# Kernel tuning notes

Hardware: AMD Instinct MI355X
Metric: run time of the kernel (lower is better)

Reference implementation:

```python
import jax, jax.numpy as jnp
import numpy as np

N, E, G = 50000, 800000, 1000
F, FM, L, H, T = 128, 16, 7, 128, 12
DIN, DH = 2 * F + 1, 2 * (2 * F + 1)  # 257, 514
UIN, UH = F + FM, 2 * F               # 144, 256

def swish(x):
    return x * jax.nn.sigmoid(x)

def setup_inputs() -> dict:
    key = jax.random.key(0)
    ks = jax.random.split(key, 16)
    pos = jax.random.normal(ks[0], (N, 3), dtype=jnp.float32)
    zi = jax.random.randint(ks[1], (N,), 0, 5)
    z = jnp.array([1, 6, 7, 8, 9], dtype=jnp.int64)[zi]  # valid atomic numbers
    edge_index = jax.random.randint(ks[2], (2, E), 0, N)
    batch = jnp.sort(jax.random.randint(ks[3], (N,), 0, G))
    def w(k, shape, fan_in):
        return jax.random.normal(k, shape, dtype=jnp.float32) / np.sqrt(fan_in)
    return {
        'pos': pos, 'z': z, 'edge_index': edge_index, 'batch': batch,
        'emb': jax.random.normal(ks[4], (5, F), dtype=jnp.float32),
        'W_msg1': w(ks[5], (L, DIN, DH), DIN), 'b_msg1': jnp.zeros((L, DH), jnp.float32),
        'W_msg2': w(ks[6], (L, DH, FM), DH), 'b_msg2': jnp.zeros((L, FM), jnp.float32),
        'W_up1': w(ks[7], (L, UIN, UH), UIN), 'b_up1': jnp.zeros((L, UH), jnp.float32),
        'W_up2': w(ks[8], (L, UH, F), UH), 'b_up2': jnp.zeros((L, F), jnp.float32),
        'Wp1': w(ks[9], (F, H), F), 'bp1': jnp.zeros((H,), jnp.float32),
        'Wp2': w(ks[10], (H, H), H), 'bp2': jnp.zeros((H,), jnp.float32),
        'Wr1': w(ks[11], (H, H), H), 'br1': jnp.zeros((H,), jnp.float32),
        'Wr2': w(ks[12], (H, T), H), 'br2': jnp.zeros((T,), jnp.float32),
        'n_graphs': G,
    }

def reference(pos, z, edge_index, batch, emb, W_msg1, b_msg1, W_msg2, b_msg2,
              W_up1, b_up1, W_up2, b_up2, Wp1, bp1, Wp2, bp2, Wr1, br1, Wr2, br2,
              n_graphs):
    n = pos.shape[0]
    atomic = jnp.array([-1, 0, -1, -1, -1, -1, 1, 2, 3, 4])
    h = emb[atomic[z]]                                  # [N, F]
    src, dst = edge_index[0], edge_index[1]
    d = pos[src] - pos[dst]
    norm2 = jnp.sum(d * d, axis=1)                      # [E] squared distance
    for l in range(W_msg1.shape[0]):
        inp = jnp.concatenate([h[dst], h[src], norm2[:, None]], axis=1)  # x_i, x_j, norm2
        m = swish(inp @ W_msg1[l] + b_msg1[l])
        m = swish(m @ W_msg2[l] + b_msg2[l])            # [E, FM]
        agg = jax.ops.segment_sum(m, dst, num_segments=n)  # aggregate at target nodes
        u = jnp.concatenate([agg, h], axis=1)           # [N, F+FM]
        u = swish(u @ W_up1[l] + b_up1[l])
        h = u @ W_up2[l] + b_up2[l] + h                 # residual update
    proj = swish(h @ Wp1 + bp1) @ Wp2 + bp2             # node_proj
    pooled = jax.ops.segment_sum(proj, batch, num_segments=n_graphs)  # global_add_pool
    return swish(pooled @ Wr1 + br1) @ Wr2 + br2        # readout [G, T]
```

## Files before the change

kernel.cpp:

```cpp
#include <hip/hip_runtime.h>
#include <hip/hip_bf16.h>
#include <cstdint>
#include <cstddef>

typedef _Float16 h16x8 __attribute__((ext_vector_type(8)));
typedef float f32x4 __attribute__((ext_vector_type(4)));

#define NSTRIPE 4

__device__ __forceinline__ void splitf16(float v, _Float16& hi, _Float16& lo) {
    hi = (_Float16)v;
    lo = (_Float16)(v - (float)hi);
}
__device__ __forceinline__ float swish_fast(float x) {
    float e = __expf(-x);
    return x * __builtin_amdgcn_rcpf(1.0f + e);
}

__global__ void init_nodes(const int* __restrict__ z, const float* __restrict__ emb,
                           float* __restrict__ hf, _Float16* __restrict__ hhi,
                           _Float16* __restrict__ hlo, int N) {
    int tid = blockIdx.x * 256 + threadIdx.x;
    int n = tid >> 7, f = tid & 127;
    int zv = z[n];
    int idx5 = (zv == 1) ? 0 : (zv - 5);
    float v = emb[idx5 * 128 + f];
    hf[tid] = v;
    _Float16 hi, lo;
    splitf16(v, hi, lo);
    hhi[tid] = hi;
    hlo[tid] = lo;
}

__device__ __forceinline__ int edge_key(int d, int s, int N, int stripeSz) {
    return (d / stripeSz) * N + s;
}

__global__ void hist_kernel(const int* __restrict__ src, const int* __restrict__ dst,
                            int* __restrict__ hist, int E, int N, int stripeSz) {
    int e = blockIdx.x * 256 + threadIdx.x;
    if (e < E) atomicAdd(&hist[edge_key(dst[e], src[e], N, stripeSz)], 1);
}

__global__ void scan_p1(const int* __restrict__ hist, int* __restrict__ blocksum, int KN) {
    __shared__ int s[256];
    int idx = blockIdx.x * 256 + threadIdx.x;
    int v = (idx < KN) ? hist[idx] : 0;
    s[threadIdx.x] = v;
    __syncthreads();
    for (int d = 128; d > 0; d >>= 1) {
        if (threadIdx.x < d) s[threadIdx.x] += s[threadIdx.x + d];
        __syncthreads();
    }
    if (threadIdx.x == 0) blocksum[blockIdx.x] = s[0];
}

__global__ void scan_p2(int* __restrict__ blocksum, int NB) {
    __shared__ int s[1024];
    int t = threadIdx.x;
    int v = (t < NB) ? blocksum[t] : 0;
    s[t] = v;
    __syncthreads();
    for (int d = 1; d < 1024; d <<= 1) {
        int x = (t >= d) ? s[t - d] : 0;
        __syncthreads();
        s[t] += x;
        __syncthreads();
    }
    if (t < NB) blocksum[t] = s[t] - v;
}

__global__ void scan_p3(const int* __restrict__ hist, const int* __restrict__ blocksum,
                        int* __restrict__ cursor, int KN) {
    __shared__ int s[256];
    int idx = blockIdx.x * 256 + threadIdx.x;
    int v = (idx < KN) ? hist[idx] : 0;
    s[threadIdx.x] = v;
    __syncthreads();
    for (int d = 1; d < 256; d <<= 1) {
        int x = (threadIdx.x >= d) ? s[threadIdx.x - d] : 0;
        __syncthreads();
        s[threadIdx.x] += x;
        __syncthreads();
    }
    if (idx < KN) cursor[idx] = blocksum[blockIdx.x] + s[threadIdx.x] - v;
}

__global__ void scatter_kernel(const int* __restrict__ src, const int* __restrict__ dst,
                               int* __restrict__ cursor, int* __restrict__ perm,
                               int E, int N, int stripeSz) {
    int e = blockIdx.x * 256 + threadIdx.x;
    if (e < E) {
        int p = atomicAdd(&cursor[edge_key(dst[e], src[e], N, stripeSz)], 1);
        perm[p] = e;
    }
}

__global__ void reorder_kernel(const int* __restrict__ perm, const int* __restrict__ src,
                               const int* __restrict__ dst, const float* __restrict__ pos,
                               int* __restrict__ srcS, int* __restrict__ dstS,
                               float* __restrict__ n2S, int E) {
    int i = blockIdx.x * 256 + threadIdx.x;
    if (i >= E) return;
    int e = perm[i];
    int si = src[e], di = dst[e];
    srcS[i] = si;
    dstS[i] = di;
    float dx = pos[si * 3 + 0] - pos[di * 3 + 0];
    float dy = pos[si * 3 + 1] - pos[di * 3 + 1];
    float dz = pos[si * 3 + 2] - pos[di * 3 + 2];
    n2S[i] = dx * dx + dy * dy + dz * dz;
}

__global__ void pack_msg1(const float* __restrict__ Wm1l, const float* __restrict__ bm1l,
                          const float* __restrict__ Wm2l,
                          _Float16* __restrict__ Bp1, float* __restrict__ bias1088,
                          _Float16* __restrict__ w1c, _Float16* __restrict__ W2p) {
    int t = blockIdx.x * 256 + threadIdx.x;
    int i = t & 7;
    int lane = (t >> 3) & 63;
    int rest = t >> 9;
    int cb = rest % 68;
    int ks = rest / 68;
    int k = ks * 32 + ((lane >> 4) << 3) + i;
    int ch = cb * 16 + (lane & 15);
    float val;
    if (ch < 544) {
        val = (ch < 514) ? Wm1l[k * 514 + ch] : 0.f;
    } else {
        int c = ch - 544;
        val = (c < 514) ? Wm1l[(128 + k) * 514 + c] : 0.f;
    }
    Bp1[t] = (_Float16)val;
    if (t < 1088) bias1088[t] = (t < 514) ? bm1l[t] : 0.f;
    if (t < 544) w1c[t] = (_Float16)((t < 514) ? Wm1l[256 * 514 + t] : 0.f);
    if (t < 8704) {
        int i2 = t & 7, lane2 = (t >> 3) & 63, ks2 = t >> 9;
        int k2 = ks2 * 32 + ((lane2 >> 4) << 3) + i2;
        int c2 = lane2 & 15;
        W2p[t] = (_Float16)((k2 < 514) ? Wm2l[k2 * 16 + c2] : 0.f);
    }
}

__global__ void pack_generic(const float* __restrict__ W, int K, int Nc,
                             _Float16* __restrict__ Bp) {
    int t = blockIdx.x * 256 + threadIdx.x;
    int i = t & 7;
    int lane = (t >> 3) & 63;
    int rest = t >> 9;
    int CB = Nc >> 4;
    int cb = rest % CB;
    int ks = rest / CB;
    int k = ks * 32 + ((lane >> 4) << 3) + i;
    int c = cb * 16 + (lane & 15);
    float val = (k < K) ? W[(size_t)k * Nc + c] : 0.f;
    Bp[t] = (_Float16)val;
}

__global__ __launch_bounds__(256) void tab_gemm(
    const _Float16* __restrict__ Ahi, const _Float16* __restrict__ Alo,
    const _Float16* __restrict__ Bp, const float* __restrict__ bias,
    _Float16* __restrict__ TA, _Float16* __restrict__ TB, int N) {
    int lane = threadIdx.x & 63;
    int wid = threadIdx.x >> 6;
    int row0 = blockIdx.x * 64 + wid * 16;
    if (row0 >= N) return;
    const size_t arow = (size_t)(row0 + (lane & 15)) * 128;
    const int ak = (lane >> 4) * 8;
    h16x8 ah[4], al[4];
#pragma unroll
    for (int ks = 0; ks < 4; ++ks) {
        ah[ks] = *(const h16x8*)(Ahi + arow + ks * 32 + ak);
        al[ks] = *(const h16x8*)(Alo + arow + ks * 32 + ak);
    }
    int col16 = lane & 15;
    int rb = (lane >> 4) * 4;
    for (int cb = 0; cb < 68; ++cb) {
        f32x4 acc = {0.f, 0.f, 0.f, 0.f};
#pragma unroll
        for (int ks = 0; ks < 4; ++ks) {
            h16x8 bh = *(const h16x8*)(Bp + ((size_t)(ks * 68 + cb) * 64 + lane) * 8);
            acc = __builtin_amdgcn_mfma_f32_16x16x32_f16(ah[ks], bh, acc, 0, 0, 0);
            acc = __builtin_amdgcn_mfma_f32_16x16x32_f16(al[ks], bh, acc, 0, 0, 0);
        }
        int col = cb * 16 + col16;
        float bv = bias[col];
        if (cb < 34) {
#pragma unroll
            for (int i = 0; i < 4; ++i)
                TA[(size_t)(row0 + rb + i) * 544 + col] = (_Float16)(acc[i] + bv);
        } else {
#pragma unroll
            for (int i = 0; i < 4; ++i)
                TB[(size_t)(row0 + rb + i) * 544 + (col - 544)] = (_Float16)(acc[i] + bv);
        }
    }
}

template <int KS, int CB, int MODE>
__global__ __launch_bounds__(256) void gemmA(
    const _Float16* __restrict__ Ahi, const _Float16* __restrict__ Alo, int lda,
    const _Float16* __restrict__ Bp, const float* __restrict__ bias,
    _Float16* __restrict__ outB, _Float16* __restrict__ outB2, int ldoB,
    float* __restrict__ outF, int ldoF, const float* __restrict__ resid,
    const int* __restrict__ batch, float* __restrict__ pooled, int N) {
    int lane = threadIdx.x & 63;
    int wid = threadIdx.x >> 6;
    int row0 = blockIdx.x * 64 + wid * 16;
    if (row0 >= N) return;
    const size_t arow = (size_t)(row0 + (lane & 15)) * lda;
    const int ak = (lane >> 4) * 8;
    h16x8 ah[KS], al[KS];
#pragma unroll
    for (int ks = 0; ks < KS; ++ks) {
        ah[ks] = *(const h16x8*)(Ahi + arow + ks * 32 + ak);
        al[ks] = *(const h16x8*)(Alo + arow + ks * 32 + ak);
    }
    int col16 = lane & 15;
    int rb = (lane >> 4) * 4;
    for (int cb = 0; cb < CB; ++cb) {
        f32x4 acc = {0.f, 0.f, 0.f, 0.f};
#pragma unroll
        for (int ks = 0; ks < KS; ++ks) {
            h16x8 bh = *(const h16x8*)(Bp + ((size_t)(ks * CB + cb) * 64 + lane) * 8);
            acc = __builtin_amdgcn_mfma_f32_16x16x32_f16(ah[ks], bh, acc, 0, 0, 0);
            acc = __builtin_amdgcn_mfma_f32_16x16x32_f16(al[ks], bh, acc, 0, 0, 0);
        }
        int col = cb * 16 + col16;
        float bv = bias[col];
#pragma unroll
        for (int i = 0; i < 4; ++i) {
            int row = row0 + rb + i;
            float v = acc[i] + bv;
            if (MODE == 1) {
                float s = swish_fast(v);
                _Float16 hi, lo;
                splitf16(s, hi, lo);
                outB[(size_t)row * ldoB + col] = hi;
                outB2[(size_t)row * ldoB + col] = lo;
            } else if (MODE == 2) {
                float h = v + resid[(size_t)row * ldoF + col];
                outF[(size_t)row * ldoF + col] = h;
                _Float16 hi, lo;
                splitf16(h, hi, lo);
                outB[(size_t)row * ldoB + col] = hi;
                outB2[(size_t)row * ldoB + col] = lo;
            } else {
                unsafeAtomicAdd(&pooled[(size_t)batch[row] * 128 + col], v);
            }
        }
    }
}

__global__ __launch_bounds__(256) void up1_gemm(
    const float* __restrict__ agg, const float* __restrict__ hf,
    const _Float16* __restrict__ Bp, const float* __restrict__ bias,
    _Float16* __restrict__ uhi, _Float16* __restrict__ ulo, int N) {
    int lane = threadIdx.x & 63;
    int wid = threadIdx.x >> 6;
    int row0 = blockIdx.x * 64 + wid * 16;
    if (row0 >= N) return;
    int r = row0 + (lane & 15);
    const int ak = (lane >> 4) * 8;
    h16x8 ah[5], al[5];
#pragma unroll
    for (int ks = 0; ks < 5; ++ks) {
        int c0 = ks * 32 + ak;
        f32x4 v0, v1;
        if (c0 < 16) {
            v0 = *(const f32x4*)(agg + (size_t)r * 16 + c0);
            v1 = *(const f32x4*)(agg + (size_t)r * 16 + c0 + 4);
        } else if (c0 < 144) {
            v0 = *(const f32x4*)(hf + (size_t)r * 128 + c0 - 16);
            v1 = *(const f32x4*)(hf + (size_t)r * 128 + c0 - 12);
        } else {
            v0 = f32x4{0.f, 0.f, 0.f, 0.f};
            v1 = f32x4{0.f, 0.f, 0.f, 0.f};
        }
        h16x8 hi8, lo8;
#pragma unroll
        for (int jj = 0; jj < 8; ++jj) {
            float x = (jj < 4) ? v0[jj] : v1[jj - 4];
            _Float16 h, l;
            splitf16(x, h, l);
            hi8[jj] = h;
            lo8[jj] = l;
        }
        ah[ks] = hi8;
        al[ks] = lo8;
    }
    int col16 = lane & 15;
    int rb = (lane >> 4) * 4;
    for (int cb = 0; cb < 16; ++cb) {
        f32x4 acc = {0.f, 0.f, 0.f, 0.f};
#pragma unroll
        for (int ks = 0; ks < 5; ++ks) {
            h16x8 bh = *(const h16x8*)(Bp + ((size_t)(ks * 16 + cb) * 64 + lane) * 8);
            acc = __builtin_amdgcn_mfma_f32_16x16x32_f16(ah[ks], bh, acc, 0, 0, 0);
            acc = __builtin_amdgcn_mfma_f32_16x16x32_f16(al[ks], bh, acc, 0, 0, 0);
        }
        int col = cb * 16 + col16;
        float bv = bias[col];
#pragma unroll
        for (int i = 0; i < 4; ++i) {
            int row = row0 + rb + i;
            float s = swish_fast(acc[i] + bv);
            _Float16 hi, lo;
            splitf16(s, hi, lo);
            uhi[(size_t)row * 256 + col] = hi;
            ulo[(size_t)row * 256 + col] = lo;
        }
    }
}

__global__ __launch_bounds__(256) void edge_kernel(
    const _Float16* __restrict__ TA, const _Float16* __restrict__ TB,
    const _Float16* __restrict__ w1c, const _Float16* __restrict__ W2p,
    const float* __restrict__ bm2l,
    const int* __restrict__ srcS, const int* __restrict__ dstS,
    const float* __restrict__ n2S, float* __restrict__ agg) {
    __shared__ _Float16 sW[8704];
    __shared__ _Float16 sw1[544];
    for (int t = threadIdx.x; t < 1088; t += 256)
        ((h16x8*)sW)[t] = ((const h16x8*)W2p)[t];
    for (int t = threadIdx.x; t < 544; t += 256) sw1[t] = w1c[t];
    __syncthreads();

    int lane = threadIdx.x & 63;
    int wid = threadIdx.x >> 6;
    int ebase = blockIdx.x * 128 + wid * 32;
    int rr = lane & 15;
    int e0 = ebase + rr;
    int e1 = ebase + 16 + rr;
    int di0 = dstS[e0], si0 = srcS[e0];
    int di1 = dstS[e1], si1 = srcS[e1];
    _Float16 n20 = (_Float16)n2S[e0];
    _Float16 n21 = (_Float16)n2S[e1];
    const int ak = (lane >> 4) * 8;
    const _Float16* pa0 = TA + (size_t)di0 * 544 + ak;
    const _Float16* pb0 = TB + (size_t)si0 * 544 + ak;
    const _Float16* pa1 = TA + (size_t)di1 * 544 + ak;
    const _Float16* pb1 = TB + (size_t)si1 * 544 + ak;

    const _Float16 nl2e = (_Float16)(-1.44269504f);
    f32x4 acc0 = {0.f, 0.f, 0.f, 0.f};
    f32x4 acc1 = {0.f, 0.f, 0.f, 0.f};

    h16x8 bufA[16], bufB[16], bufT[4];

    auto issue4 = [&](h16x8* buf, int K) {
#pragma unroll
        for (int q = 0; q < 4; ++q) {
            buf[q * 4 + 0] = *(const h16x8*)(pa0 + (K + q) * 32);
            buf[q * 4 + 1] = *(const h16x8*)(pb0 + (K + q) * 32);
            buf[q * 4 + 2] = *(const h16x8*)(pa1 + (K + q) * 32);
            buf[q * 4 + 3] = *(const h16x8*)(pb1 + (K + q) * 32);
        }
    };
    auto step = [&](const h16x8* buf, int q, int ks) {
        h16x8 va0 = buf[q * 4 + 0], vb0 = buf[q * 4 + 1];
        h16x8 va1 = buf[q * 4 + 2], vb1 = buf[q * 4 + 3];
        h16x8 wv = *(const h16x8*)(sw1 + ks * 32 + ak);
        h16x8 x0 = va0 + vb0 + wv * n20;
        h16x8 ev0 = __builtin_elementwise_exp2(x0 * nl2e);
        h16x8 d0 = ev0 + (_Float16)1.0f;
        h16x8 r0;
#pragma unroll
        for (int j = 0; j < 8; ++j) r0[j] = __builtin_amdgcn_rcph(d0[j]);
        h16x8 m0 = x0 * r0;
        h16x8 x1 = va1 + vb1 + wv * n21;
        h16x8 ev1 = __builtin_elementwise_exp2(x1 * nl2e);
        h16x8 d1 = ev1 + (_Float16)1.0f;
        h16x8 r1;
#pragma unroll
        for (int j = 0; j < 8; ++j) r1[j] = __builtin_amdgcn_rcph(d1[j]);
        h16x8 m1 = x1 * r1;
        h16x8 bh = *(const h16x8*)(sW + (ks * 64 + lane) * 8);
        acc0 = __builtin_amdgcn_mfma_f32_16x16x32_f16(m0, bh, acc0, 0, 0, 0);
        acc1 = __builtin_amdgcn_mfma_f32_16x16x32_f16(m1, bh, acc1, 0, 0, 0);
    };

    issue4(bufA, 0);
    __builtin_amdgcn_sched_barrier(0);
    issue4(bufB, 4);
    __builtin_amdgcn_sched_barrier(0);
#pragma unroll
    for (int q = 0; q < 4; ++q) step(bufA, q, q);
    issue4(bufA, 8);
    __builtin_amdgcn_sched_barrier(0);
#pragma unroll
    for (int q = 0; q < 4; ++q) step(bufB, q, 4 + q);
    issue4(bufB, 12);
    __builtin_amdgcn_sched_barrier(0);
#pragma unroll
    for (int q = 0; q < 4; ++q) step(bufA, q, 8 + q);
    bufT[0] = *(const h16x8*)(pa0 + 16 * 32);
    bufT[1] = *(const h16x8*)(pb0 + 16 * 32);
    bufT[2] = *(const h16x8*)(pa1 + 16 * 32);
    bufT[3] = *(const h16x8*)(pb1 + 16 * 32);
    __builtin_amdgcn_sched_barrier(0);
#pragma unroll
    for (int q = 0; q < 4; ++q) step(bufB, q, 12 + q);
    step(bufT, 0, 16);

    int col = lane & 15;
    float b2 = bm2l[col];
#pragma unroll
    for (int i = 0; i < 4; ++i) {
        int ea = ebase + (lane >> 4) * 4 + i;
        float v0 = swish_fast(acc0[i] + b2);
        unsafeAtomicAdd(&agg[(size_t)dstS[ea] * 16 + col], v0);
        int eb = ea + 16;
        float v1 = swish_fast(acc1[i] + b2);
        unsafeAtomicAdd(&agg[(size_t)dstS[eb] * 16 + col], v1);
    }
}

__global__ void readout(const float* __restrict__ pooled, const float* __restrict__ Wr1,
                        const float* __restrict__ br1, const float* __restrict__ Wr2,
                        const float* __restrict__ br2, float* __restrict__ out) {
    __shared__ float row[128];
    __shared__ float tt[128];
    int g = blockIdx.x;
    int t = threadIdx.x;
    row[t] = pooled[g * 128 + t];
    __syncthreads();
    float s = br1[t];
    for (int k = 0; k < 128; ++k) s += row[k] * Wr1[k * 128 + t];
    tt[t] = swish_fast(s);
    __syncthreads();
    if (t < 12) {
        float o = br2[t];
        for (int j = 0; j < 128; ++j) o += tt[j] * Wr2[j * 12 + t];
        out[g * 12 + t] = o;
    }
}

extern "C" void kernel_launch(void* const* d_in, const int* in_sizes, int n_in,
                              void* d_out, int out_size, void* d_ws, size_t ws_size,
                              hipStream_t stream) {
    const float* pos = (const float*)d_in[0];
    const int* z = (const int*)d_in[1];
    const int* ei = (const int*)d_in[2];
    const int* batch = (const int*)d_in[3];
    const float* emb = (const float*)d_in[4];
    const float* Wm1 = (const float*)d_in[5];
    const float* bm1 = (const float*)d_in[6];
    const float* Wm2 = (const float*)d_in[7];
    const float* bm2 = (const float*)d_in[8];
    const float* Wu1 = (const float*)d_in[9];
    const float* bu1 = (const float*)d_in[10];
    const float* Wu2 = (const float*)d_in[11];
    const float* bu2 = (const float*)d_in[12];
    const float* Wp1 = (const float*)d_in[13];
    const float* bp1v = (const float*)d_in[14];
    const float* Wp2 = (const float*)d_in[15];
    const float* bp2v = (const float*)d_in[16];
    const float* Wr1 = (const float*)d_in[17];
    const float* br1 = (const float*)d_in[18];
    const float* Wr2 = (const float*)d_in[19];
    const float* br2 = (const float*)d_in[20];

    const int N = in_sizes[0] / 3;
    const int E = in_sizes[2] / 2;
    const int G = out_size / 12;
    const int* src = ei;
    const int* dstp = ei + E;
    const int stripeSz = (N + NSTRIPE - 1) / NSTRIPE;
    const int KN = NSTRIPE * N;
    const int NB = (KN + 255) / 256;

    char* ws = (char*)d_ws;
    size_t off = 0;
    auto alloc = [&](size_t bytes) -> char* {
        char* p = ws + off;
        off += (bytes + 255) & ~(size_t)255;
        return p;
    };
    _Float16* TA = (_Float16*)alloc((size_t)N * 544 * 2);
    _Float16* TB = (_Float16*)alloc((size_t)N * 544 * 2);
    float* hf = (float*)alloc((size_t)N * 128 * 4);
    _Float16* hhi = (_Float16*)alloc((size_t)N * 128 * 2);
    _Float16* hlo = (_Float16*)alloc((size_t)N * 128 * 2);
    float* agg = (float*)alloc((size_t)N * 16 * 4);
    float* pooled = (float*)alloc((size_t)G * 128 * 4);
    int* hist = (int*)alloc((size_t)KN * 4);
    int* cursor = (int*)alloc((size_t)KN * 4);
    int* blocksum = (int*)alloc((size_t)NB * 4);
    int* perm = (int*)alloc((size_t)E * 4);
    int* srcS = (int*)alloc((size_t)E * 4);
    int* dstS = (int*)alloc((size_t)E * 4);
    float* n2S = (float*)alloc((size_t)E * 4);
    _Float16* Bp1 = (_Float16*)alloc(139264 * 2);
    float* bias1088 = (float*)alloc(1088 * 4);
    _Float16* w1c = (_Float16*)alloc(544 * 2);
    _Float16* W2p = (_Float16*)alloc(8704 * 2);
    _Float16* BpU1 = (_Float16*)alloc(40960 * 2);
    _Float16* BpU2 = (_Float16*)alloc(32768 * 2);
    _Float16* BpP1 = (_Float16*)alloc(16384 * 2);
    _Float16* BpP2 = (_Float16*)alloc(16384 * 2);

    _Float16* uhi = TA;
    _Float16* ulo = TA + (size_t)N * 256;
    _Float16* t1hi = TB;
    _Float16* t1lo = TB + (size_t)N * 128;

    init_nodes<<<(N * 128) / 256, 256, 0, stream>>>(z, emb, hf, hhi, hlo, N);

    hipMemsetAsync(hist, 0, (size_t)KN * 4, stream);
    hist_kernel<<<(E + 255) / 256, 256, 0, stream>>>(src, dstp, hist, E, N, stripeSz);
    scan_p1<<<NB, 256, 0, stream>>>(hist, blocksum, KN);
    scan_p2<<<1, 1024, 0, stream>>>(blocksum, NB);
    scan_p3<<<NB, 256, 0, stream>>>(hist, blocksum, cursor, KN);
    scatter_kernel<<<(E + 255) / 256, 256, 0, stream>>>(src, dstp, cursor, perm, E, N, stripeSz);
    reorder_kernel<<<(E + 255) / 256, 256, 0, stream>>>(perm, src, dstp, pos, srcS, dstS, n2S, E);

    const int gA = (N + 63) / 64;
    for (int l = 0; l < 7; ++l) {
        pack_msg1<<<139264 / 256, 256, 0, stream>>>(
            Wm1 + (size_t)l * 257 * 514, bm1 + (size_t)l * 514, Wm2 + (size_t)l * 514 * 16,
            Bp1, bias1088, w1c, W2p);
        tab_gemm<<<gA, 256, 0, stream>>>(hhi, hlo, Bp1, bias1088, TA, TB, N);
        hipMemsetAsync(agg, 0, (size_t)N * 16 * 4, stream);
        edge_kernel<<<E / 128, 256, 0, stream>>>(TA, TB, w1c, W2p, bm2 + l * 16,
                                                 srcS, dstS, n2S, agg);
        pack_generic<<<(160 * 256) / 256, 256, 0, stream>>>(
            Wu1 + (size_t)l * 144 * 256, 144, 256, BpU1);
        up1_gemm<<<gA, 256, 0, stream>>>(agg, hf, BpU1, bu1 + l * 256, uhi, ulo, N);
        pack_generic<<<(256 * 128) / 256, 256, 0, stream>>>(
            Wu2 + (size_t)l * 256 * 128, 256, 128, BpU2);
        gemmA<8, 8, 2><<<gA, 256, 0, stream>>>(
            uhi, ulo, 256, BpU2, bu2 + l * 128,
            hhi, hlo, 128, hf, 128, hf, nullptr, nullptr, N);
    }

    pack_generic<<<(128 * 128) / 256, 256, 0, stream>>>(Wp1, 128, 128, BpP1);
    gemmA<4, 8, 1><<<gA, 256, 0, stream>>>(
        hhi, hlo, 128, BpP1, bp1v,
        t1hi, t1lo, 128, nullptr, 0, nullptr, nullptr, nullptr, N);
    pack_generic<<<(128 * 128) / 256, 256, 0, stream>>>(Wp2, 128, 128, BpP2);
    hipMemsetAsync(pooled, 0, (size_t)G * 128 * 4, stream);
    gemmA<4, 8, 3><<<gA, 256, 0, stream>>>(
        t1hi, t1lo, 128, BpP2, bp2v,
        nullptr, nullptr, 0, nullptr, 0, nullptr, batch, pooled, N);
    readout<<<G, 128, 0, stream>>>(pooled, Wr1, br1, Wr2, br2, (float*)d_out);
}
```

Baseline: 2.263 ms.

## Batch weight packing for all layers upfront and fuse agg zeroing into tab_gemm

```diff
diff --git a/kernel.cpp b/kernel.cpp
--- a/kernel.cpp
+++ b/kernel.cpp
@@ -6,7 +6,7 @@
 typedef _Float16 h16x8 __attribute__((ext_vector_type(8)));
 typedef float f32x4 __attribute__((ext_vector_type(4)));
 
-#define NSTRIPE 4
+#define NSTRIPE 2
 
 __device__ __forceinline__ void splitf16(float v, _Float16& hi, _Float16& lo) {
     hi = (_Float16)v;
@@ -112,10 +112,19 @@
     n2S[i] = dx * dx + dy * dy + dz * dz;
 }
 
-__global__ void pack_msg1(const float* __restrict__ Wm1l, const float* __restrict__ bm1l,
-                          const float* __restrict__ Wm2l,
-                          _Float16* __restrict__ Bp1, float* __restrict__ bias1088,
-                          _Float16* __restrict__ w1c, _Float16* __restrict__ W2p) {
+__global__ void pack_msg1(const float* __restrict__ Wm1, const float* __restrict__ bm1,
+                          const float* __restrict__ Wm2,
+                          _Float16* __restrict__ Bp1A, float* __restrict__ biasA,
+                          _Float16* __restrict__ w1cA, _Float16* __restrict__ W2pA) {
+    int l = blockIdx.y;
+    const float* Wm1l = Wm1 + (size_t)l * 257 * 514;
+    const float* bm1l = bm1 + (size_t)l * 514;
+    const float* Wm2l = Wm2 + (size_t)l * 514 * 16;
+    _Float16* Bp1 = Bp1A + (size_t)l * 139264;
+    float* bias1088 = biasA + (size_t)l * 1088;
+    _Float16* w1c = w1cA + (size_t)l * 544;
+    _Float16* W2p = W2pA + (size_t)l * 8704;
+
     int t = blockIdx.x * 256 + threadIdx.x;
     int i = t & 7;
     int lane = (t >> 3) & 63;
@@ -142,8 +151,11 @@
     }
 }
 
-__global__ void pack_generic(const float* __restrict__ W, int K, int Nc,
-                             _Float16* __restrict__ Bp) {
+__global__ void pack_generic(const float* __restrict__ Wall, size_t strideW, int K, int Nc,
+                             _Float16* __restrict__ BpAll, size_t strideB) {
+    int l = blockIdx.y;
+    const float* W = Wall + (size_t)l * strideW;
+    _Float16* Bp = BpAll + (size_t)l * strideB;
     int t = blockIdx.x * 256 + threadIdx.x;
     int i = t & 7;
     int lane = (t >> 3) & 63;
@@ -160,7 +172,15 @@
 __global__ __launch_bounds__(256) void tab_gemm(
     const _Float16* __restrict__ Ahi, const _Float16* __restrict__ Alo,
     const _Float16* __restrict__ Bp, const float* __restrict__ bias,
-    _Float16* __restrict__ TA, _Float16* __restrict__ TB, int N) {
+    _Float16* __restrict__ TA, _Float16* __restrict__ TB, float* __restrict__ agg, int N) {
+    {
+        int base = blockIdx.x * 1024 + threadIdx.x;
+#pragma unroll
+        for (int q = 0; q < 4; ++q) {
+            int idx = base + q * 256;
+            if (idx < N * 16) agg[idx] = 0.f;
+        }
+    }
     int lane = threadIdx.x & 63;
     int wid = threadIdx.x >> 6;
     int row0 = blockIdx.x * 64 + wid * 16;
@@ -491,12 +511,12 @@
     int* srcS = (int*)alloc((size_t)E * 4);
     int* dstS = (int*)alloc((size_t)E * 4);
     float* n2S = (float*)alloc((size_t)E * 4);
-    _Float16* Bp1 = (_Float16*)alloc(139264 * 2);
-    float* bias1088 = (float*)alloc(1088 * 4);
-    _Float16* w1c = (_Float16*)alloc(544 * 2);
-    _Float16* W2p = (_Float16*)alloc(8704 * 2);
-    _Float16* BpU1 = (_Float16*)alloc(40960 * 2);
-    _Float16* BpU2 = (_Float16*)alloc(32768 * 2);
+    _Float16* Bp1A = (_Float16*)alloc((size_t)7 * 139264 * 2);
+    float* biasA = (float*)alloc((size_t)7 * 1088 * 4);
+    _Float16* w1cA = (_Float16*)alloc((size_t)7 * 544 * 2);
+    _Float16* W2pA = (_Float16*)alloc((size_t)7 * 8704 * 2);
+    _Float16* BpU1A = (_Float16*)alloc((size_t)7 * 40960 * 2);
+    _Float16* BpU2A = (_Float16*)alloc((size_t)7 * 32768 * 2);
     _Float16* BpP1 = (_Float16*)alloc(16384 * 2);
     _Float16* BpP2 = (_Float16*)alloc(16384 * 2);
 
@@ -515,30 +535,29 @@
     scatter_kernel<<<(E + 255) / 256, 256, 0, stream>>>(src, dstp, cursor, perm, E, N, stripeSz);
     reorder_kernel<<<(E + 255) / 256, 256, 0, stream>>>(perm, src, dstp, pos, srcS, dstS, n2S, E);
 
+    pack_msg1<<<dim3(139264 / 256, 7), 256, 0, stream>>>(Wm1, bm1, Wm2, Bp1A, biasA, w1cA, W2pA);
+    pack_generic<<<dim3(160, 7), 256, 0, stream>>>(Wu1, (size_t)144 * 256, 144, 256, BpU1A, 40960);
+    pack_generic<<<dim3(128, 7), 256, 0, stream>>>(Wu2, (size_t)256 * 128, 256, 128, BpU2A, 32768);
+    pack_generic<<<dim3(64, 1), 256, 0, stream>>>(Wp1, 0, 128, 128, BpP1, 0);
+    pack_generic<<<dim3(64, 1), 256, 0, stream>>>(Wp2, 0, 128, 128, BpP2, 0);
+
     const int gA = (N + 63) / 64;
     for (int l = 0; l < 7; ++l) {
-        pack_msg1<<<139264 / 256, 256, 0, stream>>>(
-            Wm1 + (size_t)l * 257 * 514, bm1 + (size_t)l * 514, Wm2 + (size_t)l * 514 * 16,
-            Bp1, bias1088, w1c, W2p);
-        tab_gemm<<<gA, 256, 0, stream>>>(hhi, hlo, Bp1, bias1088, TA, TB, N);
-        hipMemsetAsync(agg, 0, (size_t)N * 16 * 4, stream);
-        edge_kernel<<<E / 128, 256, 0, stream>>>(TA, TB, w1c, W2p, bm2 + l * 16,
+        tab_gemm<<<gA, 256, 0, stream>>>(hhi, hlo, Bp1A + (size_t)l * 139264,
+                                         biasA + (size_t)l * 1088, TA, TB, agg, N);
+        edge_kernel<<<E / 128, 256, 0, stream>>>(TA, TB, w1cA + (size_t)l * 544,
+                                                 W2pA + (size_t)l * 8704, bm2 + l * 16,
                                                  srcS, dstS, n2S, agg);
-        pack_generic<<<(160 * 256) / 256, 256, 0, stream>>>(
-            Wu1 + (size_t)l * 144 * 256, 144, 256, BpU1);
-        up1_gemm<<<gA, 256, 0, stream>>>(agg, hf, BpU1, bu1 + l * 256, uhi, ulo, N);
-        pack_generic<<<(256 * 128) / 256, 256, 0, stream>>>(
-            Wu2 + (size_t)l * 256 * 128, 256, 128, BpU2);
+        up1_gemm<<<gA, 256, 0, stream>>>(agg, hf, BpU1A + (size_t)l * 40960,
+                                         bu1 + l * 256, uhi, ulo, N);
         gemmA<8, 8, 2><<<gA, 256, 0, stream>>>(
-            uhi, ulo, 256, BpU2, bu2 + l * 128,
+            uhi, ulo, 256, BpU2A + (size_t)l * 32768, bu2 + l * 128,
             hhi, hlo, 128, hf, 128, hf, nullptr, nullptr, N);
     }
 
-    pack_generic<<<(128 * 128) / 256, 256, 0, stream>>>(Wp1, 128, 128, BpP1);
     gemmA<4, 8, 1><<<gA, 256, 0, stream>>>(
         hhi, hlo, 128, BpP1, bp1v,
         t1hi, t1lo, 128, nullptr, 0, nullptr, nullptr, nullptr, N);
-    pack_generic<<<(128 * 128) / 256, 256, 0, stream>>>(Wp2, 128, 128, BpP2);
     hipMemsetAsync(pooled, 0, (size_t)G * 128 * 4, stream);
     gemmA<4, 8, 3><<<gA, 256, 0, stream>>>(
         t1hi, t1lo, 128, BpP2, bp2v,
```

New measurement: 2.179 ms. 1.04x faster.
